# Optimization experiments

Hardware: AMD Instinct MI355X
Metric: run time of the kernel (lower is better)

Reference implementation:

```python
import jax, jax.numpy as jnp
import numpy as np

DIM = 96
SHIFT_SIZE = 3
EPS = 1e-5


def conv1x1(x, w, b):
    # x: [B,C,H,W], w: [O,C], b: [O]
    return jnp.einsum('bchw,oc->bohw', x, w) + b[None, :, None, None]


def group_norm1(x, gamma, beta):
    # GroupNorm with 1 group: normalize over (C,H,W) per sample
    mean = jnp.mean(x, axis=(1, 2, 3), keepdims=True)
    var = jnp.var(x, axis=(1, 2, 3), keepdims=True)
    xn = (x - mean) * jax.lax.rsqrt(var + EPS)
    return xn * gamma[None, :, None, None] + beta[None, :, None, None]


def axial_shift(x, shift_size, axis, sign=1):
    # pad -> chunk channels -> roll each chunk -> cat -> narrow (zero-fill shift)
    B, C, H, W = x.shape
    p = shift_size // 2
    xp = jnp.pad(x, ((0, 0), (0, 0), (p, p), (p, p)))
    chunks = jnp.split(xp, shift_size, axis=1)
    rolled = [jnp.roll(c, sign * s, axis=axis) for c, s in zip(chunks, range(-p, p + 1))]
    xc = jnp.concatenate(rolled, axis=1)
    return xc[:, :, p:p + H, p:p + W]


def setup_inputs() -> dict:
    key = jax.random.key(0)
    ks = jax.random.split(key, 13)
    B, C, H, W = 4, DIM, 256, 256
    s = 1.0 / np.sqrt(C)
    inp = {
        'x': jax.random.normal(ks[0], (B, C, H, W), jnp.float32),
        'w1': jax.random.uniform(ks[1], (C, C), jnp.float32, -s, s),
        'b1': jax.random.uniform(ks[2], (C,), jnp.float32, -s, s),
        'w21': jax.random.uniform(ks[3], (C, C), jnp.float32, -s, s),
        'b21': jax.random.uniform(ks[4], (C,), jnp.float32, -s, s),
        'w22': jax.random.uniform(ks[5], (C, C), jnp.float32, -s, s),
        'b22': jax.random.uniform(ks[6], (C,), jnp.float32, -s, s),
        'w3': jax.random.uniform(ks[7], (C, C), jnp.float32, -s, s),
        'b3': jax.random.uniform(ks[8], (C,), jnp.float32, -s, s),
        'gn1_w': jnp.ones((C,), jnp.float32),
        'gn1_b': jnp.zeros((C,), jnp.float32),
        'gn2_w': jnp.ones((C,), jnp.float32),
        'gn2_b': jnp.zeros((C,), jnp.float32),
    }
    return inp


def reference(x, w1, b1, w21, b21, w22, b22, w3, b3, gn1_w, gn1_b, gn2_w, gn2_b):
    gelu = lambda t: jax.nn.gelu(t, approximate=False)  # torch nn.GELU default (erf)
    x = gelu(group_norm1(conv1x1(x, w1, b1), gn1_w, gn1_b))
    x_lr = axial_shift(x, SHIFT_SIZE, axis=3)
    x_l_diag = axial_shift(x_lr, SHIFT_SIZE, axis=2)
    x_td = axial_shift(x, SHIFT_SIZE, axis=2)
    x_r_diag = axial_shift(x_td, SHIFT_SIZE, axis=3, sign=-1)
    out = (gelu(conv1x1(x_lr, w21, b21)) + gelu(conv1x1(x_l_diag, w21, b21))
           + gelu(conv1x1(x_td, w22, b22)) + gelu(conv1x1(x_r_diag, w22, b22)))
    out = group_norm1(out, gn2_w, gn2_b)
    return conv1x1(out, w3, b3)
```

## Files before the change

### kernel.cpp

```cpp
#include <hip/hip_runtime.h>
#include <hip/hip_bf16.h>
#include <math.h>


#define B_ 4
#define C_ 96
#define H_ 256
#define W_ 256
#define NPIX (H_ * W_)
#define GN_N ((float)(C_ * NPIX))
#define CPAD 104
#define WFRAG 9216

#define HT 8
#define WT 16
#define HHT (HT + 2)
#define HWT (WT + 2)
#define HALO_PX (HHT * HWT)
#define GR_PX 12
#define ROW_GR (HWT * GR_PX)
#define TOT_GR (HHT * ROW_GR)

typedef __attribute__((ext_vector_type(4))) float f32x4;
typedef __attribute__((ext_vector_type(8))) short short8;
typedef __attribute__((ext_vector_type(2))) unsigned int uint2v;
typedef __attribute__((ext_vector_type(4))) unsigned int uint4v;

__device__ __forceinline__ float bf2f(unsigned short u) {
    return __uint_as_float(((unsigned int)u) << 16);
}
__device__ __forceinline__ unsigned short f2bf(float v) {
    unsigned int u = __float_as_uint(v);
    unsigned int r = (u + 0x7FFFu + ((u >> 16) & 1u)) >> 16;
    return (unsigned short)r;
}
__device__ __forceinline__ unsigned int cvtpk(float lo, float hi) {
    unsigned int r;
    asm("v_cvt_pk_bf16_f32 %0, %1, %2" : "=v"(r) : "v"(lo), "v"(hi));
    return r;
}

__device__ __forceinline__ float gelu_f(float v) {
    float e = __builtin_amdgcn_exp2f(v * -2.455467f);
    return v * __builtin_amdgcn_rcpf(e + 1.0f);
}

__device__ __forceinline__ float waveReduceSum(float v) {
#pragma unroll
    for (int off = 32; off > 0; off >>= 1) v += __shfl_down(v, off);
    return v;
}

__device__ __forceinline__ f32x4 mfma16(short8 a, short8 b, f32x4 c) {
    return __builtin_amdgcn_mfma_f32_16x16x32_bf16(a, b, c, 0, 0, 0);
}

__device__ __forceinline__ short8 wfrag(const unsigned short* __restrict__ wf,
                                        int mt, int kb, int l) {
    return *reinterpret_cast<const short8*>(wf + (((mt * 3 + kb) << 6) + l) * 8);
}

__global__ void k0_prep(const float* __restrict__ w1, const float* __restrict__ w21,
                        const float* __restrict__ w22,
                        unsigned short* __restrict__ wf, float* __restrict__ stats) {
    int t = blockIdx.x * 256 + threadIdx.x;
    if (blockIdx.x == 0 && threadIdx.x < 16) stats[threadIdx.x] = 0.f;
    if (t >= 3 * WFRAG) return;
    int m = t / WFRAG, rm = t - m * WFRAG;
    int f = rm >> 3, j = rm & 7;
    int mt = f / 192, rem = f - mt * 192;
    int kb = rem >> 6, l = rem & 63;
    int row = mt * 16 + (l & 15);
    int col = kb * 32 + ((l >> 4) << 3) + j;
    const float* src = (m == 0) ? w1 : (m == 1) ? w21 : w22;
    wf[t] = f2bf(src[row * C_ + col]);
}

__global__ __launch_bounds__(256, 3) void k1_conv1(
    const float* __restrict__ x, const unsigned short* __restrict__ w1f,
    const float* __restrict__ b1, unsigned short* __restrict__ ap,
    float* __restrict__ stats) {
    __shared__ unsigned short xs[256 * CPAD];
    __shared__ float red[8];
    int tid = threadIdx.x;
    int b = blockIdx.x >> 8;
    int h = blockIdx.x & 255;
    int pix0 = h << 8;
    size_t xbase = (size_t)b * C_ * NPIX + pix0 + tid;
    int lb = tid * CPAD;
#pragma unroll
    for (int c0 = 0; c0 < C_; c0 += 8) {
        float f[8];
#pragma unroll
        for (int j = 0; j < 8; ++j) f[j] = x[xbase + (size_t)(c0 + j) * NPIX];
        uint4v pk = {cvtpk(f[0], f[1]), cvtpk(f[2], f[3]),
                     cvtpk(f[4], f[5]), cvtpk(f[6], f[7])};
        *reinterpret_cast<uint4v*>(&xs[lb + c0]) = pk;
    }
    __syncthreads();
    int l = tid & 63, wv = tid >> 6;
    int bx = l & 15, q = l >> 4, cl = q * 8;
    short8 bfr[4][3];
#pragma unroll
    for (int nf = 0; nf < 4; ++nf) {
        int p = (4 * wv + nf) * 16 + bx;
#pragma unroll
        for (int kb = 0; kb < 3; ++kb)
            bfr[nf][kb] = *reinterpret_cast<const short8*>(&xs[p * CPAD + kb * 32 + cl]);
    }
    unsigned int* xsu = reinterpret_cast<unsigned int*>(xs);
    float ls = 0.f, lsq = 0.f;
    for (int mt = 0; mt < 6; ++mt) {
        int m0 = mt * 16;
        short8 af[3];
#pragma unroll
        for (int kb = 0; kb < 3; ++kb) af[kb] = wfrag(w1f, mt, kb, l);
        f32x4 acc[4];
#pragma unroll
        for (int nf = 0; nf < 4; ++nf) acc[nf] = (f32x4){0.f, 0.f, 0.f, 0.f};
#pragma unroll
        for (int nf = 0; nf < 4; ++nf)
#pragma unroll
            for (int kb = 0; kb < 3; ++kb)
                acc[nf] = mfma16(af[kb], bfr[nf][kb], acc[nf]);
        int o = m0 + q * 4;
        float b0 = b1[o], b1v = b1[o + 1], b2v = b1[o + 2], b3v = b1[o + 3];
#pragma unroll
        for (int nf = 0; nf < 4; ++nf) {
            int p = (4 * wv + nf) * 16 + bx;
            float y0 = acc[nf][0] + b0, y1v = acc[nf][1] + b1v;
            float y2 = acc[nf][2] + b2v, y3 = acc[nf][3] + b3v;
            ls += y0 + y1v + y2 + y3;
            lsq += y0 * y0 + y1v * y1v + y2 * y2 + y3 * y3;
            xsu[p * (CPAD / 2) + (o >> 1)] = cvtpk(y0, y1v);
            xsu[p * (CPAD / 2) + (o >> 1) + 1] = cvtpk(y2, y3);
        }
    }
    __syncthreads();
    size_t abase = (size_t)(b * NPIX + pix0 + tid) * C_;
#pragma unroll
    for (int c0 = 0; c0 < C_; c0 += 8)
        *reinterpret_cast<short8*>(&ap[abase + c0]) =
            *reinterpret_cast<short8*>(&xs[tid * CPAD + c0]);
    ls = waveReduceSum(ls);
    lsq = waveReduceSum(lsq);
    if (l == 0) { red[wv] = ls; red[4 + wv] = lsq; }
    __syncthreads();
    if (tid == 0) {
        atomicAdd(&stats[b], red[0] + red[1] + red[2] + red[3]);
        atomicAdd(&stats[4 + b], red[4] + red[5] + red[6] + red[7]);
    }
}

__global__ void k2_fin(float* stats, int so, int dof) {
    int t = threadIdx.x;
    if (t < 4) {
        float mean = stats[so + t] / GN_N;
        float var = stats[so + 4 + t] / GN_N - mean * mean;
        stats[dof + t] = mean;
        stats[dof + 4 + t] = rsqrtf(var + 1e-5f);
    }
}

__global__ __launch_bounds__(256, 4) void k3_main(
    const unsigned short* __restrict__ ap,
    const unsigned short* __restrict__ w21f, const float* __restrict__ b21,
    const unsigned short* __restrict__ w22f, const float* __restrict__ b22,
    const float* __restrict__ gn1w, const float* __restrict__ gn1b,
    unsigned short* __restrict__ zb, float* __restrict__ stats) {
    __shared__ unsigned short as_t[HALO_PX * CPAD];
    __shared__ float red[8];
    __shared__ float scs[C_], offs[C_];
    int tid = threadIdx.x;
    int wseg = blockIdx.x & 15;
    int hseg = (blockIdx.x >> 4) & 31;
    int b = blockIdx.x >> 9;
    int l = tid & 63, wv = tid >> 6;
    int h0 = hseg * HT, w0 = wseg * WT;
    float m1 = stats[16 + b], r1 = stats[20 + b];
    if (tid < C_) {
        float sc = r1 * gn1w[tid];
        scs[tid] = sc;
        offs[tid] = gn1b[tid] - m1 * sc;
    }
    __syncthreads();
    for (int g = tid; g < TOT_GR; g += 256) {
        int row = g / ROW_GR;
        int rem = g - row * ROW_GR;
        int p = rem / GR_PX;
        int cgr = rem - p * GR_PX;
        int hh = h0 - 1 + row, ww = w0 - 1 + p;
        unsigned short* dst = &as_t[(row * HWT + p) * CPAD + cgr * 8];
        if (((unsigned)hh < (unsigned)H_) && ((unsigned)ww < (unsigned)W_)) {
            short8 raw = *reinterpret_cast<const short8*>(
                &ap[(size_t)(b * NPIX + hh * W_ + ww) * C_ + cgr * 8]);
            float gv[8];
#pragma unroll
            for (int j = 0; j < 8; ++j) {
                int c = cgr * 8 + j;
                gv[j] = gelu_f(fmaf(bf2f((unsigned short)raw[j]), scs[c], offs[c]));
            }
            uint4v pk = {cvtpk(gv[0], gv[1]), cvtpk(gv[2], gv[3]),
                         cvtpk(gv[4], gv[5]), cvtpk(gv[6], gv[7])};
            *reinterpret_cast<uint4v*>(dst) = pk;
        } else {
            *reinterpret_cast<uint4v*>(dst) = (uint4v){0, 0, 0, 0};
        }
    }
    __syncthreads();
    int bx = l & 15, q = l >> 4, cl = q * 8;
    int Xb = (bx + 1) * CPAD + cl;
#define FR(R, dx, kb) (*reinterpret_cast<const short8*>( \
        &as_t[((R)*HWT + (dx)) * CPAD + Xb + (kb)*32]))
    float ls = 0.f, lsq = 0.f;
#pragma unroll
    for (int nf = 0; nf < 2; ++nf) {
        int r = 2 * wv + nf;
        short8 f0a = FR(r + 1, 1, 0), f0b = FR(r + 2, 1, 0);
        short8 f0c = FR(r + 2, 0, 0), f0d = FR(r + 2, -1, 0);
        short8 fC = FR(r + 1, 0, 1);
        short8 f2a = FR(r + 1, -1, 2), f2b = FR(r, -1, 2);
        short8 f2c = FR(r, 0, 2), f2d = FR(r, 1, 2);
        size_t zpix = (size_t)(b * NPIX + (h0 + r) * W_ + w0 + bx) * C_;
        for (int mt = 0; mt < 6; ++mt) {
            int m0 = mt * 16;
            short8 aA0 = wfrag(w21f, mt, 0, l);
            short8 aA1 = wfrag(w21f, mt, 1, l);
            short8 aA2 = wfrag(w21f, mt, 2, l);
            short8 aB0 = wfrag(w22f, mt, 0, l);
            short8 aB1 = wfrag(w22f, mt, 1, l);
            short8 aB2 = wfrag(w22f, mt, 2, l);
            const f32x4 bb1 = *reinterpret_cast<const f32x4*>(&b21[m0 + q * 4]);
            const f32x4 bb2 = *reinterpret_cast<const f32x4*>(&b22[m0 + q * 4]);
            f32x4 a0 = bb1, a1 = bb1, a2 = bb2, a3 = bb2;
            a0 = mfma16(aA0, f0a, a0);
            a1 = mfma16(aA0, f0b, a1);
            a2 = mfma16(aB0, f0c, a2);
            a3 = mfma16(aB0, f0d, a3);
            a0 = mfma16(aA1, fC, a0);
            a1 = mfma16(aA1, fC, a1);
            a2 = mfma16(aB1, fC, a2);
            a3 = mfma16(aB1, fC, a3);
            a0 = mfma16(aA2, f2a, a0);
            a1 = mfma16(aA2, f2b, a1);
            a2 = mfma16(aB2, f2c, a2);
            a3 = mfma16(aB2, f2d, a3);
            float zv[4];
#pragma unroll
            for (int rg = 0; rg < 4; ++rg) {
                float z0 = gelu_f(a0[rg]) + gelu_f(a1[rg]) +
                           gelu_f(a2[rg]) + gelu_f(a3[rg]);
                zv[rg] = z0;
                ls += z0;
                lsq += z0 * z0;
            }
            uint2v pk;
            pk.x = cvtpk(zv[0], zv[1]);
            pk.y = cvtpk(zv[2], zv[3]);
            *reinterpret_cast<uint2v*>(&zb[zpix + m0 + q * 4]) = pk;
        }
    }
#undef FR
    ls = waveReduceSum(ls);
    lsq = waveReduceSum(lsq);
    if (l == 0) { red[wv] = ls; red[4 + wv] = lsq; }
    __syncthreads();
    if (tid == 0) {
        atomicAdd(&stats[8 + b], red[0] + red[1] + red[2] + red[3]);
        atomicAdd(&stats[12 + b], red[4] + red[5] + red[6] + red[7]);
    }
}

__global__ void k4b_fold(const float* __restrict__ w3, const float* __restrict__ b3,
                         const float* __restrict__ gn2w, const float* __restrict__ gn2b,
                         const float* __restrict__ stats,
                         unsigned short* __restrict__ w3pf, float* __restrict__ b3p) {
    int b = blockIdx.x;
    int t = threadIdx.x;
    float mean = stats[8 + b] / GN_N;
    float var = stats[12 + b] / GN_N - mean * mean;
    float r2 = rsqrtf(var + 1e-5f);
#pragma unroll
    for (int k = 0; k < 36; ++k) {
        int idx = t + k * 256;
        int f = idx >> 3, j = idx & 7;
        int mt = f / 192, rem = f - mt * 192;
        int kb = rem >> 6, l = rem & 63;
        int row = mt * 16 + (l & 15);
        int col = kb * 32 + ((l >> 4) << 3) + j;
        float sc = r2 * gn2w[col];
        w3pf[(size_t)b * WFRAG + idx] = f2bf(w3[row * C_ + col] * sc);
    }
    if (t < C_) {
        float acc = 0.f;
        for (int c = 0; c < C_; ++c) {
            float sc = r2 * gn2w[c];
            float off = gn2b[c] - mean * sc;
            acc = fmaf(w3[t * C_ + c], off, acc);
        }
        b3p[b * C_ + t] = acc + b3[t];
    }
}

__global__ __launch_bounds__(256, 3) void k5_conv3(
    const unsigned short* __restrict__ zb,
    const unsigned short* __restrict__ w3pf, const float* __restrict__ b3p,
    float* __restrict__ out) {
    __shared__ unsigned short zs[256 * CPAD];
    int tid = threadIdx.x;
    int b = blockIdx.x >> 8;
    int pix0 = (blockIdx.x & 255) << 8;
    {
        const short8* src = reinterpret_cast<const short8*>(
            &zb[(size_t)(b * NPIX + pix0 + tid) * C_]);
        int lb = tid * CPAD;
#pragma unroll
        for (int i = 0; i < 12; ++i)
            *reinterpret_cast<short8*>(&zs[lb + i * 8]) = src[i];
    }
    __syncthreads();
    int l = tid & 63, wv = tid >> 6;
    int bx = l & 15, q = l >> 4, cl = q * 8;
    short8 bfr[4][3];
#pragma unroll
    for (int nf = 0; nf < 4; ++nf) {
        int p = (4 * wv + nf) * 16 + bx;
#pragma unroll
        for (int kb = 0; kb < 3; ++kb)
            bfr[nf][kb] = *reinterpret_cast<const short8*>(&zs[p * CPAD + kb * 32 + cl]);
    }
    const unsigned short* wbase = w3pf + (size_t)b * WFRAG;
    const float* bb = b3p + b * C_;
    for (int mt = 0; mt < 6; ++mt) {
        int m0 = mt * 16;
        short8 af0 = wfrag(wbase, mt, 0, l);
        short8 af1 = wfrag(wbase, mt, 1, l);
        short8 af2 = wfrag(wbase, mt, 2, l);
        f32x4 acc[4];
#pragma unroll
        for (int nf = 0; nf < 4; ++nf) acc[nf] = (f32x4){0.f, 0.f, 0.f, 0.f};
#pragma unroll
        for (int nf = 0; nf < 4; ++nf) {
            acc[nf] = mfma16(af0, bfr[nf][0], acc[nf]);
            acc[nf] = mfma16(af1, bfr[nf][1], acc[nf]);
            acc[nf] = mfma16(af2, bfr[nf][2], acc[nf]);
        }
        int o = m0 + q * 4;
        float b0 = bb[o], b1v = bb[o + 1], b2v = bb[o + 2], b3v = bb[o + 3];
#pragma unroll
        for (int nf = 0; nf < 4; ++nf) {
            int p = pix0 + (4 * wv + nf) * 16 + bx;
            size_t ob0 = (size_t)(b * C_ + o) * NPIX + p;
            out[ob0] = acc[nf][0] + b0;
            out[ob0 + NPIX] = acc[nf][1] + b1v;
            out[ob0 + 2 * NPIX] = acc[nf][2] + b2v;
            out[ob0 + 3 * NPIX] = acc[nf][3] + b3v;
        }
    }
}

extern "C" void kernel_launch(void* const* d_in, const int* in_sizes, int n_in,
                              void* d_out, int out_size, void* d_ws, size_t ws_size,
                              hipStream_t stream) {
    const float* x = (const float*)d_in[0];
    const float* w1 = (const float*)d_in[1];
    const float* b1 = (const float*)d_in[2];
    const float* w21 = (const float*)d_in[3];
    const float* b21 = (const float*)d_in[4];
    const float* w22 = (const float*)d_in[5];
    const float* b22 = (const float*)d_in[6];
    const float* w3 = (const float*)d_in[7];
    const float* b3 = (const float*)d_in[8];
    const float* gn1w = (const float*)d_in[9];
    const float* gn1b = (const float*)d_in[10];
    const float* gn2w = (const float*)d_in[11];
    const float* gn2b = (const float*)d_in[12];
    float* out = (float*)d_out;
    char* ws = (char*)d_ws;

    const size_t NB = (size_t)B_ * NPIX * C_ * sizeof(unsigned short);
    unsigned short* ap = (unsigned short*)ws;
    unsigned short* zb = (unsigned short*)(ws + NB);
    float* stats = (float*)(ws + 2 * NB);
    unsigned short* wf = (unsigned short*)(ws + 2 * NB + 128);
    unsigned short* w1f = wf;
    unsigned short* w21f = wf + WFRAG;
    unsigned short* w22f = wf + 2 * WFRAG;
    unsigned short* w3pf = wf + 3 * WFRAG;
    float* b3p = (float*)(w3pf + B_ * WFRAG);

    hipLaunchKernelGGL(k0_prep, dim3(112), dim3(256), 0, stream,
                       w1, w21, w22, wf, stats);
    hipLaunchKernelGGL(k1_conv1, dim3(1024), dim3(256), 0, stream, x, w1f, b1, ap, stats);
    hipLaunchKernelGGL(k2_fin, dim3(1), dim3(64), 0, stream, stats, 0, 16);
    hipLaunchKernelGGL(k3_main, dim3(2048), dim3(256), 0, stream,
                       ap, w21f, b21, w22f, b22, gn1w, gn1b, zb, stats);
    hipLaunchKernelGGL(k4b_fold, dim3(B_), dim3(256), 0, stream,
                       w3, b3, gn2w, gn2b, stats, w3pf, b3p);
    hipLaunchKernelGGL(k5_conv3, dim3(1024), dim3(256), 0, stream,
                       zb, w3pf, b3p, out);
}
```

Measured before the change: 166.6 us.

## Split GN1+GELU into separate pass and double-buffer halo tiles via direct LDS loads

The GroupNorm1 affine and GELU are moved out of the main shift-conv kernel into a new in-place elementwise pass over the intermediate activations. The main kernel then processes four width tiles per block and stages each halo tile straight into LDS with global_load_lds, double-buffered so the next tile loads while the current one runs MFMAs. Out-of-range halo pixels read from a small zeroed buffer set up in the prep kernel. This removes the duplicated per-halo GELU work and the register round trip on loads, at the cost of an extra full read/write pass over the activation tensor and fewer, larger blocks.

```diff
diff --git a/kernel.cpp b/kernel.cpp
--- a/kernel.cpp
+++ b/kernel.cpp
@@ -16,10 +16,12 @@
 #define WT 16
 #define HHT (HT + 2)
 #define HWT (WT + 2)
-#define HALO_PX (HHT * HWT)
-#define GR_PX 12
+#define GR_PX 13
 #define ROW_GR (HWT * GR_PX)
 #define TOT_GR (HHT * ROW_GR)
+#define NLD 10
+#define BUFG 2432
+#define TPB 4
 
 typedef __attribute__((ext_vector_type(4))) float f32x4;
 typedef __attribute__((ext_vector_type(8))) short short8;
@@ -62,9 +64,12 @@
 
 __global__ void k0_prep(const float* __restrict__ w1, const float* __restrict__ w21,
                         const float* __restrict__ w22,
-                        unsigned short* __restrict__ wf, float* __restrict__ stats) {
+                        unsigned short* __restrict__ wf, float* __restrict__ stats,
+                        unsigned short* __restrict__ zpg) {
     int t = blockIdx.x * 256 + threadIdx.x;
     if (blockIdx.x == 0 && threadIdx.x < 16) stats[threadIdx.x] = 0.f;
+    if (blockIdx.x == 0 && threadIdx.x >= 16 && threadIdx.x < 144)
+        zpg[threadIdx.x - 16] = 0;
     if (t >= 3 * WFRAG) return;
     int m = t / WFRAG, rm = t - m * WFRAG;
     int f = rm >> 3, j = rm & 7;
@@ -162,21 +167,13 @@
     }
 }
 
-__global__ __launch_bounds__(256, 4) void k3_main(
-    const unsigned short* __restrict__ ap,
-    const unsigned short* __restrict__ w21f, const float* __restrict__ b21,
-    const unsigned short* __restrict__ w22f, const float* __restrict__ b22,
-    const float* __restrict__ gn1w, const float* __restrict__ gn1b,
-    unsigned short* __restrict__ zb, float* __restrict__ stats) {
-    __shared__ unsigned short as_t[HALO_PX * CPAD];
-    __shared__ float red[8];
+__global__ __launch_bounds__(256) void k2b_gelu(
+    unsigned short* __restrict__ ap, const float* __restrict__ gn1w,
+    const float* __restrict__ gn1b, const float* __restrict__ stats) {
     __shared__ float scs[C_], offs[C_];
     int tid = threadIdx.x;
-    int wseg = blockIdx.x & 15;
-    int hseg = (blockIdx.x >> 4) & 31;
-    int b = blockIdx.x >> 9;
-    int l = tid & 63, wv = tid >> 6;
-    int h0 = hseg * HT, w0 = wseg * WT;
+    int b = blockIdx.x >> 8;
+    int pix = ((blockIdx.x & 255) << 8) + tid;
     float m1 = stats[16 + b], r1 = stats[20 + b];
     if (tid < C_) {
         float sc = r1 * gn1w[tid];
@@ -184,83 +181,132 @@
         offs[tid] = gn1b[tid] - m1 * sc;
     }
     __syncthreads();
-    for (int g = tid; g < TOT_GR; g += 256) {
-        int row = g / ROW_GR;
-        int rem = g - row * ROW_GR;
-        int p = rem / GR_PX;
-        int cgr = rem - p * GR_PX;
-        int hh = h0 - 1 + row, ww = w0 - 1 + p;
-        unsigned short* dst = &as_t[(row * HWT + p) * CPAD + cgr * 8];
-        if (((unsigned)hh < (unsigned)H_) && ((unsigned)ww < (unsigned)W_)) {
-            short8 raw = *reinterpret_cast<const short8*>(
-                &ap[(size_t)(b * NPIX + hh * W_ + ww) * C_ + cgr * 8]);
-            float gv[8];
-#pragma unroll
-            for (int j = 0; j < 8; ++j) {
-                int c = cgr * 8 + j;
-                gv[j] = gelu_f(fmaf(bf2f((unsigned short)raw[j]), scs[c], offs[c]));
+    size_t base = (size_t)(b * NPIX + pix) * C_;
+#pragma unroll
+    for (int i = 0; i < 12; ++i) {
+        short8 v = *reinterpret_cast<const short8*>(&ap[base + i * 8]);
+        float gv[8];
+#pragma unroll
+        for (int j = 0; j < 8; ++j) {
+            int c = i * 8 + j;
+            gv[j] = gelu_f(fmaf(bf2f((unsigned short)v[j]), scs[c], offs[c]));
+        }
+        uint4v pk = {cvtpk(gv[0], gv[1]), cvtpk(gv[2], gv[3]),
+                     cvtpk(gv[4], gv[5]), cvtpk(gv[6], gv[7])};
+        *reinterpret_cast<uint4v*>(&ap[base + i * 8]) = pk;
+    }
+}
+
+__global__ __launch_bounds__(256, 2) void k3_main(
+    const unsigned short* __restrict__ ap, const unsigned short* __restrict__ zpg,
+    const unsigned short* __restrict__ w21f, const float* __restrict__ b21,
+    const unsigned short* __restrict__ w22f, const float* __restrict__ b22,
+    unsigned short* __restrict__ zb, float* __restrict__ stats) {
+    __shared__ unsigned short asb[2][BUFG * 8];
+    __shared__ float red[8];
+    int tid = threadIdx.x;
+    int l = tid & 63, wv = tid >> 6;
+    int wg = blockIdx.x & 3;
+    int hseg = (blockIdx.x >> 2) & 31;
+    int b = blockIdx.x >> 7;
+    int h0 = hseg * HT;
+    const unsigned short* apb = ap + (size_t)b * NPIX * C_;
+    int bx = l & 15, q = l >> 4, cl = q * 8;
+    float ls = 0.f, lsq = 0.f;
+
+    auto stage = [&](int bf, int tile) {
+        int w0 = (wg * 4 + tile) * WT;
+#pragma unroll
+        for (int k = 0; k < NLD; ++k) {
+            int i = wv + 4 * k;
+            int g = i * 64 + l;
+            unsigned ug = (unsigned)g;
+            unsigned r = ug / 234u;
+            unsigned rem = ug - r * 234u;
+            unsigned p = rem / 13u;
+            unsigned cgr = rem - p * 13u;
+            int hh = h0 - 1 + (int)r;
+            int ww = w0 - 1 + (int)p;
+            bool valid = (g < TOT_GR) && ((unsigned)hh < (unsigned)H_) &&
+                         ((unsigned)ww < (unsigned)W_) && (cgr < 12u);
+            const unsigned short* src = valid
+                ? apb + ((size_t)(((hh & 255) << 8) | (ww & 255)) * C_ + cgr * 8)
+                : zpg;
+            unsigned short* dst = &asb[bf][(i <= 36 ? i * 64 : 2368) * 8];
+            __builtin_amdgcn_global_load_lds(
+                (const __attribute__((address_space(1))) unsigned int*)src,
+                (__attribute__((address_space(3))) unsigned int*)dst, 16, 0, 0);
+        }
+    };
+
+    stage(0, 0);
+    for (int t = 0; t < TPB; ++t) {
+        int cur = t & 1;
+        if (t + 1 < TPB) {
+            stage(cur ^ 1, t + 1);
+            asm volatile("s_waitcnt vmcnt(10)" ::: "memory");
+        } else {
+            asm volatile("s_waitcnt vmcnt(0)" ::: "memory");
+        }
+        __builtin_amdgcn_sched_barrier(0);
+        __builtin_amdgcn_s_barrier();
+        __builtin_amdgcn_sched_barrier(0);
+        const unsigned short* asp = &asb[cur][0];
+        int w0 = (wg * 4 + t) * WT;
+        int Xb = (bx + 1) * CPAD + cl;
+#define FR(R, dx, kb) (*reinterpret_cast<const short8*>( \
+        &asp[((R)*HWT + (dx)) * CPAD + Xb + (kb)*32]))
+#pragma unroll
+        for (int nf = 0; nf < 2; ++nf) {
+            int r = 2 * wv + nf;
+            short8 f0a = FR(r + 1, 1, 0), f0b = FR(r + 2, 1, 0);
+            short8 f0c = FR(r + 2, 0, 0), f0d = FR(r + 2, -1, 0);
+            short8 fC = FR(r + 1, 0, 1);
+            short8 f2a = FR(r + 1, -1, 2), f2b = FR(r, -1, 2);
+            short8 f2c = FR(r, 0, 2), f2d = FR(r, 1, 2);
+            size_t zpix = (size_t)(b * NPIX + (h0 + r) * W_ + w0 + bx) * C_;
+            for (int mt = 0; mt < 6; ++mt) {
+                int m0 = mt * 16;
+                short8 aA0 = wfrag(w21f, mt, 0, l);
+                short8 aA1 = wfrag(w21f, mt, 1, l);
+                short8 aA2 = wfrag(w21f, mt, 2, l);
+                short8 aB0 = wfrag(w22f, mt, 0, l);
+                short8 aB1 = wfrag(w22f, mt, 1, l);
+                short8 aB2 = wfrag(w22f, mt, 2, l);
+                const f32x4 bb1 = *reinterpret_cast<const f32x4*>(&b21[m0 + q * 4]);
+                const f32x4 bb2 = *reinterpret_cast<const f32x4*>(&b22[m0 + q * 4]);
+                f32x4 a0 = bb1, a1 = bb1, a2 = bb2, a3 = bb2;
+                a0 = mfma16(aA0, f0a, a0);
+                a1 = mfma16(aA0, f0b, a1);
+                a2 = mfma16(aB0, f0c, a2);
+                a3 = mfma16(aB0, f0d, a3);
+                a0 = mfma16(aA1, fC, a0);
+                a1 = mfma16(aA1, fC, a1);
+                a2 = mfma16(aB1, fC, a2);
+                a3 = mfma16(aB1, fC, a3);
+                a0 = mfma16(aA2, f2a, a0);
+                a1 = mfma16(aA2, f2b, a1);
+                a2 = mfma16(aB2, f2c, a2);
+                a3 = mfma16(aB2, f2d, a3);
+                float zv[4];
+#pragma unroll
+                for (int rg = 0; rg < 4; ++rg) {
+                    float z0 = gelu_f(a0[rg]) + gelu_f(a1[rg]) +
+                               gelu_f(a2[rg]) + gelu_f(a3[rg]);
+                    zv[rg] = z0;
+                    ls += z0;
+                    lsq += z0 * z0;
+                }
+                uint2v pk;
+                pk.x = cvtpk(zv[0], zv[1]);
+                pk.y = cvtpk(zv[2], zv[3]);
+                *reinterpret_cast<uint2v*>(&zb[zpix + m0 + q * 4]) = pk;
             }
-            uint4v pk = {cvtpk(gv[0], gv[1]), cvtpk(gv[2], gv[3]),
-                         cvtpk(gv[4], gv[5]), cvtpk(gv[6], gv[7])};
-            *reinterpret_cast<uint4v*>(dst) = pk;
-        } else {
-            *reinterpret_cast<uint4v*>(dst) = (uint4v){0, 0, 0, 0};
-        }
-    }
-    __syncthreads();
-    int bx = l & 15, q = l >> 4, cl = q * 8;
-    int Xb = (bx + 1) * CPAD + cl;
-#define FR(R, dx, kb) (*reinterpret_cast<const short8*>( \
-        &as_t[((R)*HWT + (dx)) * CPAD + Xb + (kb)*32]))
-    float ls = 0.f, lsq = 0.f;
-#pragma unroll
-    for (int nf = 0; nf < 2; ++nf) {
-        int r = 2 * wv + nf;
-        short8 f0a = FR(r + 1, 1, 0), f0b = FR(r + 2, 1, 0);
-        short8 f0c = FR(r + 2, 0, 0), f0d = FR(r + 2, -1, 0);
-        short8 fC = FR(r + 1, 0, 1);
-        short8 f2a = FR(r + 1, -1, 2), f2b = FR(r, -1, 2);
-        short8 f2c = FR(r, 0, 2), f2d = FR(r, 1, 2);
-        size_t zpix = (size_t)(b * NPIX + (h0 + r) * W_ + w0 + bx) * C_;
-        for (int mt = 0; mt < 6; ++mt) {
-            int m0 = mt * 16;
-            short8 aA0 = wfrag(w21f, mt, 0, l);
-            short8 aA1 = wfrag(w21f, mt, 1, l);
-            short8 aA2 = wfrag(w21f, mt, 2, l);
-            short8 aB0 = wfrag(w22f, mt, 0, l);
-            short8 aB1 = wfrag(w22f, mt, 1, l);
-            short8 aB2 = wfrag(w22f, mt, 2, l);
-            const f32x4 bb1 = *reinterpret_cast<const f32x4*>(&b21[m0 + q * 4]);
-            const f32x4 bb2 = *reinterpret_cast<const f32x4*>(&b22[m0 + q * 4]);
-            f32x4 a0 = bb1, a1 = bb1, a2 = bb2, a3 = bb2;
-            a0 = mfma16(aA0, f0a, a0);
-            a1 = mfma16(aA0, f0b, a1);
-            a2 = mfma16(aB0, f0c, a2);
-            a3 = mfma16(aB0, f0d, a3);
-            a0 = mfma16(aA1, fC, a0);
-            a1 = mfma16(aA1, fC, a1);
-            a2 = mfma16(aB1, fC, a2);
-            a3 = mfma16(aB1, fC, a3);
-            a0 = mfma16(aA2, f2a, a0);
-            a1 = mfma16(aA2, f2b, a1);
-            a2 = mfma16(aB2, f2c, a2);
-            a3 = mfma16(aB2, f2d, a3);
-            float zv[4];
-#pragma unroll
-            for (int rg = 0; rg < 4; ++rg) {
-                float z0 = gelu_f(a0[rg]) + gelu_f(a1[rg]) +
-                           gelu_f(a2[rg]) + gelu_f(a3[rg]);
-                zv[rg] = z0;
-                ls += z0;
-                lsq += z0 * z0;
-            }
-            uint2v pk;
-            pk.x = cvtpk(zv[0], zv[1]);
-            pk.y = cvtpk(zv[2], zv[3]);
-            *reinterpret_cast<uint2v*>(&zb[zpix + m0 + q * 4]) = pk;
-        }
-    }
+        }
 #undef FR
+        __builtin_amdgcn_sched_barrier(0);
+        __builtin_amdgcn_s_barrier();
+    }
     ls = waveReduceSum(ls);
     lsq = waveReduceSum(lsq);
     if (l == 0) { red[wv] = ls; red[4 + wv] = lsq; }
@@ -382,7 +428,8 @@
     unsigned short* ap = (unsigned short*)ws;
     unsigned short* zb = (unsigned short*)(ws + NB);
     float* stats = (float*)(ws + 2 * NB);
-    unsigned short* wf = (unsigned short*)(ws + 2 * NB + 128);
+    unsigned short* zpg = (unsigned short*)(ws + 2 * NB + 128);
+    unsigned short* wf = (unsigned short*)(ws + 2 * NB + 384);
     unsigned short* w1f = wf;
     unsigned short* w21f = wf + WFRAG;
     unsigned short* w22f = wf + 2 * WFRAG;
@@ -390,11 +437,13 @@
     float* b3p = (float*)(w3pf + B_ * WFRAG);
 
     hipLaunchKernelGGL(k0_prep, dim3(112), dim3(256), 0, stream,
-                       w1, w21, w22, wf, stats);
+                       w1, w21, w22, wf, stats, zpg);
     hipLaunchKernelGGL(k1_conv1, dim3(1024), dim3(256), 0, stream, x, w1f, b1, ap, stats);
     hipLaunchKernelGGL(k2_fin, dim3(1), dim3(64), 0, stream, stats, 0, 16);
-    hipLaunchKernelGGL(k3_main, dim3(2048), dim3(256), 0, stream,
-                       ap, w21f, b21, w22f, b22, gn1w, gn1b, zb, stats);
+    hipLaunchKernelGGL(k2b_gelu, dim3(1024), dim3(256), 0, stream,
+                       ap, gn1w, gn1b, stats);
+    hipLaunchKernelGGL(k3_main, dim3(512), dim3(256), 0, stream,
+                       ap, zpg, w21f, b21, w22f, b22, zb, stats);
     hipLaunchKernelGGL(k4b_fold, dim3(B_), dim3(256), 0, stream,
                        w3, b3, gn2w, gn2b, stats, w3pf, b3p);
     hipLaunchKernelGGL(k5_conv3, dim3(1024), dim3(256), 0, stream,
```

New measurement: 195.8 us. 17.6% more time.
